# Kernel tuning notes

Measured on AMD Instinct MI355X. Metric: run time of the kernel, lower is better.

## Reference

```python
import jax, jax.numpy as jnp
import numpy as np

B, N, S, VOCAB, D, NNZ = 16, 2048, 4096, 50257, 128, 1048576


def setup_inputs() -> dict:
    key = jax.random.key(0)
    k1, k2, k3, k4, k5, k6 = jax.random.split(key, 6)
    return {
        "subnode_ids": jax.random.randint(k1, (B, S), 0, VOCAB),
        "mask_batch": jax.random.randint(k2, (NNZ,), 0, B),
        "mask_node": jax.random.randint(k3, (NNZ,), 0, N),
        "mask_subnode": jax.random.randint(k4, (NNZ,), 0, S),
        "mask_values": jax.random.uniform(k5, (NNZ,), dtype=jnp.float32),
        "emb_table": jax.random.normal(k6, (VOCAB, D), dtype=jnp.float32),
    }


def reference(subnode_ids, mask_batch, mask_node, mask_subnode, mask_values, emb_table):
    # Gather token embeddings for every (batch, subnode) slot: [B, S, D] -> [B*S, D]
    subnode_emb = emb_table[subnode_ids].reshape(B * S, D)
    # Flattened COO indices (same as batch*max_nodes + node, batch*max_subnodes + subnode)
    row = mask_batch * N + mask_node      # destination node slot in [0, B*N)
    col = mask_batch * S + mask_subnode   # source subnode slot in [0, B*S)
    # Fused gather + weighted scatter-add (== sparse.mm of expanded_mask @ subnode_emb)
    contrib = subnode_emb[col] * mask_values[:, None]           # [NNZ, D]
    pooled = jax.ops.segment_sum(contrib, row, num_segments=B * N)  # [B*N, D]
    return pooled.reshape(B, N, D)
```

## Files before the change

### kernel.cpp

```cpp
#include <hip/hip_runtime.h>
#include <hip/hip_fp16.h>

#define Bq 16
#define Nq 2048
#define Sq 4096
#define Dq 128
#define VOCABq 50257
#define NNZq 1048576
#define ROWS (Bq * Nq)
#define NBIN 2048
#define RPB 16
#define BCAP 768
#define OVF_MAX 65536
#define BTPB 1024
#define BEPT 4
#define NBBIN 256
#define CAST_QPT 4
#define CSTRIDE 16

typedef unsigned long long u64;
typedef float vfloat4 __attribute__((ext_vector_type(4)));
typedef unsigned short vushort4 __attribute__((ext_vector_type(4)));
typedef unsigned short vushort8 __attribute__((ext_vector_type(8)));

__global__ __launch_bounds__(BTPB) void cast_bin_kernel(
    const float* __restrict__ emb,
    unsigned short* __restrict__ emb16,
    const int* __restrict__ subnode_ids,
    const int* __restrict__ mb,
    const int* __restrict__ mn,
    const int* __restrict__ ms,
    const float* __restrict__ mv,
    int* __restrict__ binCnt,
    u64* __restrict__ binMem,
    int* __restrict__ ovfn,
    int* __restrict__ ovf)
{
    __shared__ int hist[NBIN];
    __shared__ int base[NBIN];
    int t = threadIdx.x;

    if (blockIdx.x >= NBBIN) {
        const int NQUAD = (VOCABq * Dq) / 4;
        int b0 = (blockIdx.x - NBBIN) * (BTPB * CAST_QPT) + t;
        #pragma unroll
        for (int k = 0; k < CAST_QPT; k++) {
            int i = b0 + k * BTPB;
            if (i < NQUAD) {
                vfloat4 f = reinterpret_cast<const vfloat4*>(emb)[i];
                vushort4 h;
                h.x = __half_as_ushort(__float2half_rn(f.x));
                h.y = __half_as_ushort(__float2half_rn(f.y));
                h.z = __half_as_ushort(__float2half_rn(f.z));
                h.w = __half_as_ushort(__float2half_rn(f.w));
                __builtin_nontemporal_store(h, reinterpret_cast<vushort4*>(emb16) + i);
            }
        }
        return;
    }

    for (int g = t; g < NBIN; g += BTPB) hist[g] = 0;
    __syncthreads();

    int blockBase = blockIdx.x * (BTPB * BEPT);
    int g[BEPT], rank[BEPT];
    u64 pk[BEPT];
    #pragma unroll
    for (int k = 0; k < BEPT; k++) {
        int i   = blockBase + k * BTPB + t;
        int b   = __builtin_nontemporal_load(mb + i);
        int row = b * Nq + __builtin_nontemporal_load(mn + i);
        int s   = __builtin_nontemporal_load(ms + i);
        float v = __builtin_nontemporal_load(mv + i);
        int tok = subnode_ids[b * Sq + s];
        g[k]  = row >> 4;
        pk[k] = ((u64)(unsigned)__float_as_int(v) << 32)
              | ((u64)(row & 15) << 16)
              | (unsigned)tok;
        rank[k] = atomicAdd(&hist[g[k]], 1);
    }
    __syncthreads();
    for (int gg = t; gg < NBIN; gg += BTPB) {
        int h = hist[gg];
        base[gg] = h ? atomicAdd(&binCnt[gg * CSTRIDE], h) : 0;
    }
    __syncthreads();
    #pragma unroll
    for (int k = 0; k < BEPT; k++) {
        int p = base[g[k]] + rank[k];
        if (p < BCAP) {
            binMem[(size_t)g[k] * BCAP + p] = pk[k];
        } else {
            int o = atomicAdd(ovfn, 1);
            if (o < OVF_MAX) ovf[o] = blockBase + k * BTPB + t;
        }
    }
}

__global__ __launch_bounds__(256) void pool_kernel(
    const unsigned short* __restrict__ emb16,
    const int* __restrict__ binCnt,
    const u64* __restrict__ binMem,
    const int* __restrict__ subnode_ids,
    const int* __restrict__ mb, const int* __restrict__ mn,
    const int* __restrict__ ms, const float* __restrict__ mv,
    const int* __restrict__ ovfn, const int* __restrict__ ovf,
    float* __restrict__ out)
{
    __shared__ u64 ebuf[BCAP];
    __shared__ int hist[64];
    __shared__ int start[65];
    __shared__ int cursor[64];

    int t   = threadIdx.x;
    int bin = blockIdx.x;
    if (t < 64) hist[t] = 0;
    __syncthreads();

    int n = min(binCnt[bin * CSTRIDE], BCAP);
    const u64* bm = binMem + (size_t)bin * BCAP;

    u64 myPk[3];
    int myKey[3], myCnt = 0;
    for (int e = t; e < n; e += 256) {
        u64 pk  = __builtin_nontemporal_load(bm + e);
        int tok = (int)(pk & 0xFFFF);
        int key = ((tok >> 14) << 4) | (int)((pk >> 16) & 15);
        myPk[myCnt] = pk; myKey[myCnt] = key; myCnt++;
        atomicAdd(&hist[key], 1);
    }
    __syncthreads();
    if (t < 64) {
        int v = hist[t];
        #pragma unroll
        for (int d = 1; d < 64; d <<= 1) {
            int w = __shfl_up(v, d, 64);
            if (t >= d) v += w;
        }
        start[t + 1] = v;
        if (t == 0) start[0] = 0;
    }
    __syncthreads();
    if (t < 64) cursor[t] = start[t];
    __syncthreads();
    for (int k = 0; k < myCnt; k++) {
        int p = atomicAdd(&cursor[myKey[k]], 1);
        ebuf[p] = myPk[k];
    }
    __syncthreads();

    int g    = t >> 4;
    int lane = t & 15;
    vfloat4 a0 = {0.f, 0.f, 0.f, 0.f};
    vfloat4 a1 = {0.f, 0.f, 0.f, 0.f};
    #pragma unroll
    for (int q = 0; q < 4; q++) {
        int s0 = start[q * 16 + g], s1 = start[q * 16 + g + 1];
        int k = s0;
        for (; k + 8 <= s1; k += 8) {
            int   tk[8];
            float vv[8];
            #pragma unroll
            for (int u = 0; u < 8; u++) {
                u64 pk = ebuf[k + u];
                tk[u] = (int)(pk & 0xFFFF);
                vv[u] = __int_as_float((int)(pk >> 32));
            }
            vushort8 e[8];
            #pragma unroll
            for (int u = 0; u < 8; u++)
                e[u] = reinterpret_cast<const vushort8*>(emb16 + (size_t)tk[u] * Dq)[lane];
            #pragma unroll
            for (int u = 0; u < 8; u++) {
                a0.x += __half2float(__ushort_as_half(e[u][0])) * vv[u];
                a0.y += __half2float(__ushort_as_half(e[u][1])) * vv[u];
                a0.z += __half2float(__ushort_as_half(e[u][2])) * vv[u];
                a0.w += __half2float(__ushort_as_half(e[u][3])) * vv[u];
                a1.x += __half2float(__ushort_as_half(e[u][4])) * vv[u];
                a1.y += __half2float(__ushort_as_half(e[u][5])) * vv[u];
                a1.z += __half2float(__ushort_as_half(e[u][6])) * vv[u];
                a1.w += __half2float(__ushort_as_half(e[u][7])) * vv[u];
            }
        }
        for (; k < s1; k++) {
            u64 pk = ebuf[k];
            int   tok = (int)(pk & 0xFFFF);
            float v   = __int_as_float((int)(pk >> 32));
            vushort8 e = reinterpret_cast<const vushort8*>(emb16 + (size_t)tok * Dq)[lane];
            a0.x += __half2float(__ushort_as_half(e[0])) * v;
            a0.y += __half2float(__ushort_as_half(e[1])) * v;
            a0.z += __half2float(__ushort_as_half(e[2])) * v;
            a0.w += __half2float(__ushort_as_half(e[3])) * v;
            a1.x += __half2float(__ushort_as_half(e[4])) * v;
            a1.y += __half2float(__ushort_as_half(e[5])) * v;
            a1.z += __half2float(__ushort_as_half(e[6])) * v;
            a1.w += __half2float(__ushort_as_half(e[7])) * v;
        }
    }

    int nov = min(*ovfn, OVF_MAX);
    for (int e2 = 0; e2 < nov; e2++) {
        int i = ovf[e2];
        int b = mb[i];
        int row = b * Nq + mn[i];
        if ((row >> 4) != bin || (row & 15) != g) continue;
        int tok = subnode_ids[b * Sq + ms[i]];
        float v = mv[i];
        vushort8 e = reinterpret_cast<const vushort8*>(emb16 + (size_t)tok * Dq)[lane];
        a0.x += __half2float(__ushort_as_half(e[0])) * v;
        a0.y += __half2float(__ushort_as_half(e[1])) * v;
        a0.z += __half2float(__ushort_as_half(e[2])) * v;
        a0.w += __half2float(__ushort_as_half(e[3])) * v;
        a1.x += __half2float(__ushort_as_half(e[4])) * v;
        a1.y += __half2float(__ushort_as_half(e[5])) * v;
        a1.z += __half2float(__ushort_as_half(e[6])) * v;
        a1.w += __half2float(__ushort_as_half(e[7])) * v;
    }

    float* orow = out + ((size_t)bin * RPB + g) * Dq + lane * 8;
    __builtin_nontemporal_store(a0, reinterpret_cast<vfloat4*>(orow));
    __builtin_nontemporal_store(a1, reinterpret_cast<vfloat4*>(orow) + 1);
}

extern "C" void kernel_launch(void* const* d_in, const int* in_sizes, int n_in,
                              void* d_out, int out_size, void* d_ws, size_t ws_size,
                              hipStream_t stream) {
    const int*   subnode_ids  = (const int*)d_in[0];
    const int*   mask_batch   = (const int*)d_in[1];
    const int*   mask_node    = (const int*)d_in[2];
    const int*   mask_subnode = (const int*)d_in[3];
    const float* mask_values  = (const float*)d_in[4];
    const float* emb_table    = (const float*)d_in[5];
    float*       out          = (float*)d_out;

    unsigned short* emb16 = (unsigned short*)d_ws;
    u64* binMem = (u64*)(emb16 + (size_t)VOCABq * Dq + 64 );
    int* binCnt = (int*)(binMem + (size_t)NBIN * BCAP);
    int* ovfn   = binCnt + NBIN * CSTRIDE;
    int* ovf    = ovfn + 64;

    (void)hipMemsetAsync(binCnt, 0, (NBIN * CSTRIDE + 64) * sizeof(int), stream);

    const int NQUAD = (VOCABq * Dq) / 4;
    const int NBCAST = (NQUAD + BTPB * CAST_QPT - 1) / (BTPB * CAST_QPT);
    cast_bin_kernel<<<NBBIN + NBCAST, BTPB, 0, stream>>>(
        emb_table, emb16, subnode_ids, mask_batch, mask_node, mask_subnode,
        mask_values, binCnt, binMem, ovfn, ovf);
    pool_kernel<<<NBIN, 256, 0, stream>>>(
        emb16, binCnt, binMem, subnode_ids, mask_batch, mask_node, mask_subnode,
        mask_values, ovfn, ovf, out);
}
```

Baseline: 148.2 us.

## Coarsen bins to 64 rows, locally sort bin entries, split cast kernel

Bins grow from 16 to 64 output rows (512 bins of capacity 2432), and the pool kernel runs 1024 threads per block with 256 sort keys. The bin kernel now does a block-wide prefix scan and stages entries in shared memory grouped by bin, so the global scatter into bin storage is written contiguously rather than as scattered 8-byte stores. The fp32-to-fp16 table cast moves into its own kernel, which also zeroes the bin counters in place of a memset. The cost is that the cast no longer overlaps with binning, and binning needs more shared memory and extra barriers.

```diff
diff --git a/kernel.cpp b/kernel.cpp
--- a/kernel.cpp
+++ b/kernel.cpp
@@ -8,24 +8,43 @@
 #define VOCABq 50257
 #define NNZq 1048576
 #define ROWS (Bq * Nq)
-#define NBIN 2048
-#define RPB 16
-#define BCAP 768
+#define NBIN 512
+#define RPB 64
+#define BCAP 2432
 #define OVF_MAX 65536
 #define BTPB 1024
 #define BEPT 4
-#define NBBIN 256
-#define CAST_QPT 4
+#define ENT (BTPB * BEPT)
+#define NBBLK (NNZq / ENT)
 #define CSTRIDE 16
+#define PTPB 1024
+#define NKEY 256
 
 typedef unsigned long long u64;
 typedef float vfloat4 __attribute__((ext_vector_type(4)));
 typedef unsigned short vushort4 __attribute__((ext_vector_type(4)));
 typedef unsigned short vushort8 __attribute__((ext_vector_type(8)));
 
-__global__ __launch_bounds__(BTPB) void cast_bin_kernel(
-    const float* __restrict__ emb,
-    unsigned short* __restrict__ emb16,
+__global__ __launch_bounds__(256) void cast_kernel(
+    const float* __restrict__ emb, unsigned short* __restrict__ emb16,
+    int* __restrict__ binCnt)
+{
+    if (blockIdx.x == 0) {
+        for (int i = threadIdx.x; i < NBIN * CSTRIDE + 64; i += 256) binCnt[i] = 0;
+    }
+    const int NQUAD = (VOCABq * Dq) / 4;
+    int i = blockIdx.x * 256 + threadIdx.x;
+    if (i >= NQUAD) return;
+    vfloat4 f = reinterpret_cast<const vfloat4*>(emb)[i];
+    vushort4 h;
+    h.x = __half_as_ushort(__float2half_rn(f.x));
+    h.y = __half_as_ushort(__float2half_rn(f.y));
+    h.z = __half_as_ushort(__float2half_rn(f.z));
+    h.w = __half_as_ushort(__float2half_rn(f.w));
+    __builtin_nontemporal_store(h, reinterpret_cast<vushort4*>(emb16) + i);
+}
+
+__global__ __launch_bounds__(BTPB) void bin_kernel(
     const int* __restrict__ subnode_ids,
     const int* __restrict__ mb,
     const int* __restrict__ mn,
@@ -37,32 +56,17 @@
     int* __restrict__ ovf)
 {
     __shared__ int hist[NBIN];
-    __shared__ int base[NBIN];
+    __shared__ int lstart[NBIN];
+    __shared__ int baseG[NBIN];
+    __shared__ int waveSum[8];
+    __shared__ u64 spk[ENT];
+    __shared__ int sdst[ENT];
+
     int t = threadIdx.x;
-
-    if (blockIdx.x >= NBBIN) {
-        const int NQUAD = (VOCABq * Dq) / 4;
-        int b0 = (blockIdx.x - NBBIN) * (BTPB * CAST_QPT) + t;
-        #pragma unroll
-        for (int k = 0; k < CAST_QPT; k++) {
-            int i = b0 + k * BTPB;
-            if (i < NQUAD) {
-                vfloat4 f = reinterpret_cast<const vfloat4*>(emb)[i];
-                vushort4 h;
-                h.x = __half_as_ushort(__float2half_rn(f.x));
-                h.y = __half_as_ushort(__float2half_rn(f.y));
-                h.z = __half_as_ushort(__float2half_rn(f.z));
-                h.w = __half_as_ushort(__float2half_rn(f.w));
-                __builtin_nontemporal_store(h, reinterpret_cast<vushort4*>(emb16) + i);
-            }
-        }
-        return;
-    }
-
-    for (int g = t; g < NBIN; g += BTPB) hist[g] = 0;
-    __syncthreads();
-
-    int blockBase = blockIdx.x * (BTPB * BEPT);
+    if (t < NBIN) hist[t] = 0;
+    __syncthreads();
+
+    int blockBase = blockIdx.x * ENT;
     int g[BEPT], rank[BEPT];
     u64 pk[BEPT];
     #pragma unroll
@@ -73,31 +77,59 @@
         int s   = __builtin_nontemporal_load(ms + i);
         float v = __builtin_nontemporal_load(mv + i);
         int tok = subnode_ids[b * Sq + s];
-        g[k]  = row >> 4;
+        g[k]  = row >> 6;
         pk[k] = ((u64)(unsigned)__float_as_int(v) << 32)
-              | ((u64)(row & 15) << 16)
+              | ((u64)(row & 63) << 16)
               | (unsigned)tok;
         rank[k] = atomicAdd(&hist[g[k]], 1);
     }
     __syncthreads();
-    for (int gg = t; gg < NBIN; gg += BTPB) {
-        int h = hist[gg];
-        base[gg] = h ? atomicAdd(&binCnt[gg * CSTRIDE], h) : 0;
-    }
-    __syncthreads();
+
+    int lane = t & 63, wid = t >> 6;
+    int v  = (t < NBIN) ? hist[t] : 0;
+    int vi = v;
+    #pragma unroll
+    for (int d = 1; d < 64; d <<= 1) {
+        int w = __shfl_up(vi, d, 64);
+        if (lane >= d) vi += w;
+    }
+    if (t < NBIN && lane == 63) waveSum[wid] = vi;
+    if (t < NBIN && v) baseG[t] = atomicAdd(&binCnt[t * CSTRIDE], v);
+    __syncthreads();
+    if (t == 0) {
+        int s = 0;
+        #pragma unroll
+        for (int w = 0; w < NBIN / 64; w++) { int x = waveSum[w]; waveSum[w] = s; s += x; }
+    }
+    __syncthreads();
+    if (t < NBIN) lstart[t] = vi - v + waveSum[wid];
+    __syncthreads();
+
     #pragma unroll
     for (int k = 0; k < BEPT; k++) {
-        int p = base[g[k]] + rank[k];
-        if (p < BCAP) {
-            binMem[(size_t)g[k] * BCAP + p] = pk[k];
+        int b = g[k], r = rank[k];
+        int p = lstart[b] + r;
+        spk[p] = pk[k];
+        int pos = baseG[b] + r;
+        if (pos < BCAP) {
+            sdst[p] = b * BCAP + pos;
         } else {
+            sdst[p] = -1;
             int o = atomicAdd(ovfn, 1);
             if (o < OVF_MAX) ovf[o] = blockBase + k * BTPB + t;
         }
     }
-}
-
-__global__ __launch_bounds__(256) void pool_kernel(
+    __syncthreads();
+
+    #pragma unroll
+    for (int k = 0; k < BEPT; k++) {
+        int p = t + k * BTPB;
+        int d = sdst[p];
+        if (d >= 0) binMem[d] = spk[p];
+    }
+}
+
+__global__ __launch_bounds__(PTPB) void pool_kernel(
     const unsigned short* __restrict__ emb16,
     const int* __restrict__ binCnt,
     const u64* __restrict__ binMem,
@@ -108,13 +140,14 @@
     float* __restrict__ out)
 {
     __shared__ u64 ebuf[BCAP];
-    __shared__ int hist[64];
-    __shared__ int start[65];
-    __shared__ int cursor[64];
+    __shared__ int hist[NKEY];
+    __shared__ int start[NKEY + 1];
+    __shared__ int cursor[NKEY];
+    __shared__ int waveSum[4];
 
     int t   = threadIdx.x;
     int bin = blockIdx.x;
-    if (t < 64) hist[t] = 0;
+    if (t < NKEY) hist[t] = 0;
     __syncthreads();
 
     int n = min(binCnt[bin * CSTRIDE], BCAP);
@@ -122,26 +155,37 @@
 
     u64 myPk[3];
     int myKey[3], myCnt = 0;
-    for (int e = t; e < n; e += 256) {
-        u64 pk  = __builtin_nontemporal_load(bm + e);
+    for (int e = t; e < n; e += PTPB) {
+        u64 pk  = bm[e];
         int tok = (int)(pk & 0xFFFF);
-        int key = ((tok >> 14) << 4) | (int)((pk >> 16) & 15);
+        int key = ((tok >> 14) << 6) | (int)((pk >> 16) & 63);
         myPk[myCnt] = pk; myKey[myCnt] = key; myCnt++;
         atomicAdd(&hist[key], 1);
     }
     __syncthreads();
-    if (t < 64) {
-        int v = hist[t];
+
+    int lane = t & 63, wid = t >> 6;
+    int v  = (t < NKEY) ? hist[t] : 0;
+    int vi = v;
+    #pragma unroll
+    for (int d = 1; d < 64; d <<= 1) {
+        int w = __shfl_up(vi, d, 64);
+        if (lane >= d) vi += w;
+    }
+    if (t < NKEY && lane == 63) waveSum[wid] = vi;
+    __syncthreads();
+    if (t == 0) {
+        int s = 0;
         #pragma unroll
-        for (int d = 1; d < 64; d <<= 1) {
-            int w = __shfl_up(v, d, 64);
-            if (t >= d) v += w;
-        }
-        start[t + 1] = v;
-        if (t == 0) start[0] = 0;
-    }
-    __syncthreads();
-    if (t < 64) cursor[t] = start[t];
+        for (int w = 0; w < NKEY / 64; w++) { int x = waveSum[w]; waveSum[w] = s; s += x; }
+    }
+    __syncthreads();
+    if (t < NKEY) {
+        int ex = vi - v + waveSum[wid];
+        start[t] = ex;
+        cursor[t] = ex;
+        if (t == NKEY - 1) start[NKEY] = ex + v;
+    }
     __syncthreads();
     for (int k = 0; k < myCnt; k++) {
         int p = atomicAdd(&cursor[myKey[k]], 1);
@@ -150,12 +194,12 @@
     __syncthreads();
 
     int g    = t >> 4;
-    int lane = t & 15;
+    int lane16 = t & 15;
     vfloat4 a0 = {0.f, 0.f, 0.f, 0.f};
     vfloat4 a1 = {0.f, 0.f, 0.f, 0.f};
     #pragma unroll
     for (int q = 0; q < 4; q++) {
-        int s0 = start[q * 16 + g], s1 = start[q * 16 + g + 1];
+        int s0 = start[q * 64 + g], s1 = start[q * 64 + g + 1];
         int k = s0;
         for (; k + 8 <= s1; k += 8) {
             int   tk[8];
@@ -169,7 +213,7 @@
             vushort8 e[8];
             #pragma unroll
             for (int u = 0; u < 8; u++)
-                e[u] = reinterpret_cast<const vushort8*>(emb16 + (size_t)tk[u] * Dq)[lane];
+                e[u] = reinterpret_cast<const vushort8*>(emb16 + (size_t)tk[u] * Dq)[lane16];
             #pragma unroll
             for (int u = 0; u < 8; u++) {
                 a0.x += __half2float(__ushort_as_half(e[u][0])) * vv[u];
@@ -185,16 +229,16 @@
         for (; k < s1; k++) {
             u64 pk = ebuf[k];
             int   tok = (int)(pk & 0xFFFF);
-            float v   = __int_as_float((int)(pk >> 32));
-            vushort8 e = reinterpret_cast<const vushort8*>(emb16 + (size_t)tok * Dq)[lane];
-            a0.x += __half2float(__ushort_as_half(e[0])) * v;
-            a0.y += __half2float(__ushort_as_half(e[1])) * v;
-            a0.z += __half2float(__ushort_as_half(e[2])) * v;
-            a0.w += __half2float(__ushort_as_half(e[3])) * v;
-            a1.x += __half2float(__ushort_as_half(e[4])) * v;
-            a1.y += __half2float(__ushort_as_half(e[5])) * v;
-            a1.z += __half2float(__ushort_as_half(e[6])) * v;
-            a1.w += __half2float(__ushort_as_half(e[7])) * v;
+            float v2  = __int_as_float((int)(pk >> 32));
+            vushort8 e = reinterpret_cast<const vushort8*>(emb16 + (size_t)tok * Dq)[lane16];
+            a0.x += __half2float(__ushort_as_half(e[0])) * v2;
+            a0.y += __half2float(__ushort_as_half(e[1])) * v2;
+            a0.z += __half2float(__ushort_as_half(e[2])) * v2;
+            a0.w += __half2float(__ushort_as_half(e[3])) * v2;
+            a1.x += __half2float(__ushort_as_half(e[4])) * v2;
+            a1.y += __half2float(__ushort_as_half(e[5])) * v2;
+            a1.z += __half2float(__ushort_as_half(e[6])) * v2;
+            a1.w += __half2float(__ushort_as_half(e[7])) * v2;
         }
     }
 
@@ -203,21 +247,21 @@
         int i = ovf[e2];
         int b = mb[i];
         int row = b * Nq + mn[i];
-        if ((row >> 4) != bin || (row & 15) != g) continue;
+        if ((row >> 6) != bin || (row & 63) != g) continue;
         int tok = subnode_ids[b * Sq + ms[i]];
-        float v = mv[i];
-        vushort8 e = reinterpret_cast<const vushort8*>(emb16 + (size_t)tok * Dq)[lane];
-        a0.x += __half2float(__ushort_as_half(e[0])) * v;
-        a0.y += __half2float(__ushort_as_half(e[1])) * v;
-        a0.z += __half2float(__ushort_as_half(e[2])) * v;
-        a0.w += __half2float(__ushort_as_half(e[3])) * v;
-        a1.x += __half2float(__ushort_as_half(e[4])) * v;
-        a1.y += __half2float(__ushort_as_half(e[5])) * v;
-        a1.z += __half2float(__ushort_as_half(e[6])) * v;
-        a1.w += __half2float(__ushort_as_half(e[7])) * v;
-    }
-
-    float* orow = out + ((size_t)bin * RPB + g) * Dq + lane * 8;
+        float v2 = mv[i];
+        vushort8 e = reinterpret_cast<const vushort8*>(emb16 + (size_t)tok * Dq)[lane16];
+        a0.x += __half2float(__ushort_as_half(e[0])) * v2;
+        a0.y += __half2float(__ushort_as_half(e[1])) * v2;
+        a0.z += __half2float(__ushort_as_half(e[2])) * v2;
+        a0.w += __half2float(__ushort_as_half(e[3])) * v2;
+        a1.x += __half2float(__ushort_as_half(e[4])) * v2;
+        a1.y += __half2float(__ushort_as_half(e[5])) * v2;
+        a1.z += __half2float(__ushort_as_half(e[6])) * v2;
+        a1.w += __half2float(__ushort_as_half(e[7])) * v2;
+    }
+
+    float* orow = out + ((size_t)bin * RPB + g) * Dq + lane16 * 8;
     __builtin_nontemporal_store(a0, reinterpret_cast<vfloat4*>(orow));
     __builtin_nontemporal_store(a1, reinterpret_cast<vfloat4*>(orow) + 1);
 }
@@ -239,14 +283,12 @@
     int* ovfn   = binCnt + NBIN * CSTRIDE;
     int* ovf    = ovfn + 64;
 
-    (void)hipMemsetAsync(binCnt, 0, (NBIN * CSTRIDE + 64) * sizeof(int), stream);
-
     const int NQUAD = (VOCABq * Dq) / 4;
-    const int NBCAST = (NQUAD + BTPB * CAST_QPT - 1) / (BTPB * CAST_QPT);
-    cast_bin_kernel<<<NBBIN + NBCAST, BTPB, 0, stream>>>(
-        emb_table, emb16, subnode_ids, mask_batch, mask_node, mask_subnode,
-        mask_values, binCnt, binMem, ovfn, ovf);
-    pool_kernel<<<NBIN, 256, 0, stream>>>(
+    cast_kernel<<<(NQUAD + 255) / 256, 256, 0, stream>>>(emb_table, emb16, binCnt);
+    bin_kernel<<<NBBLK, BTPB, 0, stream>>>(
+        subnode_ids, mask_batch, mask_node, mask_subnode, mask_values,
+        binCnt, binMem, ovfn, ovf);
+    pool_kernel<<<NBIN, PTPB, 0, stream>>>(
         emb16, binCnt, binMem, subnode_ids, mask_batch, mask_node, mask_subnode,
         mask_values, ovfn, ovf, out);
 }
```

Result: faster. 131.3 us (-11.4%).
